# Optimization experiments

Measured on AMD Instinct MI355X. Metric: run time of the kernel, lower is better.

## Reference

```python
import jax, jax.numpy as jnp
import numpy as np

B, L, K1, P = 16, 224, 8192, 16  # batch, spectral bands, pixels, endmembers
LEAKY_SLOPE = 0.01  # torch nn.LeakyReLU default


def setup_inputs() -> dict:
    key = jax.random.key(0)
    ks = jax.random.split(key, 7)
    return {
        "a": jax.random.normal(ks[0], (B, P, K1), jnp.float32),
        "d2": jax.random.normal(ks[1], (B, P, K1), jnp.float32),
        "y": jax.random.normal(ks[2], (B, L, K1), jnp.float32),
        "w3_w": jax.random.normal(ks[3], (P, P), jnp.float32) * 0.1,  # Conv1d(P,P,1) weight squeezed
        "b3_w": jax.random.normal(ks[4], (P, P), jnp.float32) * 0.1,
        "w3_c": jax.random.normal(ks[5], (1, L, P), jnp.float32),     # kernel codebook
        "sigma": jnp.ones((1,), jnp.float32) * 2.0,
        "ca_w": jax.random.normal(ks[6], (2, P), jnp.float32) * 0.1,  # CA Conv1d(P,2,1) weight squeezed
    }


def reference(a, d2, y, w3_w, b3_w, w3_c, sigma, ca_w):
    # h2 = Conv1d(P,P,1)(a - d2)  -> pointwise matmul over channel dim
    h2 = jnp.einsum('pq,bqn->bpn', w3_w, a - d2)  # (B,P,K1)

    # GaussianKernelLayer: pairwise L2 distances between y pixels (B,L,K1)
    # and codebook columns w3_c (1,L,P), via the GEMM identity
    # ||u-v||^2 = ||u||^2 + ||v||^2 - 2 u.v  (avoids the (B,L,K1,P) broadcast).
    y_sq = jnp.sum(y * y, axis=1)            # (B,K1)
    c_sq = jnp.sum(w3_c * w3_c, axis=1)      # (1,P)
    cross = jnp.einsum('blk,olp->bkp', y, w3_c)  # (B,K1,P)
    dist_sq = jnp.maximum(y_sq[:, :, None] + c_sq[:, None, :] - 2.0 * cross, 0.0)
    dist = jnp.sqrt(dist_sq)                 # (B,K1,P)
    h3 = jnp.exp(-0.5 * jnp.square(dist / sigma[0]))
    h3 = jnp.transpose(h3, (0, 2, 1))        # (B,P,K1)

    # CA channel attention: avg/max pool over pixels -> Conv1d(P,2,1) -> LeakyReLU -> softmax
    avg = jnp.mean(h3, axis=-1)              # (B,P)
    mx = jnp.max(h3, axis=-1)                # (B,P)
    conv_lrelu = lambda v: jax.nn.leaky_relu(jnp.einsum('cp,bp->bc', ca_w, v), LEAKY_SLOPE)
    ratio = jax.nn.softmax(conv_lrelu(avg) + conv_lrelu(mx), axis=-1)  # (B,2)

    # combine center pixel + mean pixel via bmm with ratio
    mid = h3[:, :, K1 // 2]                  # (B,P)
    mean = jnp.mean(h3, axis=-1)             # (B,P)
    stacked = jnp.stack([mid, mean], axis=1)  # (B,2,P)
    comb = jnp.einsum('bc,bcp->bp', ratio, stacked)  # (B,P)

    # h4 = Conv1d(P,P,1)(comb[:, :, None])
    h4 = jnp.einsum('pq,bq->bp', b3_w, comb)[:, :, None]  # (B,P,1)

    return h4 + h2  # broadcast over pixel dim -> (B,P,K1)
```

## Files before the change

kernel.cpp:

```cpp
#include <hip/hip_runtime.h>

#define Bn  16
#define Ln  224
#define K1n 8192
#define Pn  16
#define NCHUNK 16
#define RG  16
#define NG  (Ln / RG)


__global__ __launch_bounds__(512, 2) void k_stats(
    const float* __restrict__ y,
    const float* __restrict__ w3c,
    const float* __restrict__ sigma,
    float* __restrict__ ws_sum,
    float* __restrict__ ws_max,
    float* __restrict__ ws_mid)
{
    __shared__ float s_csq_part[32][Pn];
    __shared__ float s_csq[Pn];
    __shared__ float s_part_s[8][Pn];
    __shared__ float s_part_m[8][Pn];

    const int tid   = threadIdx.x;
    const int lane  = tid & 63;
    const int wv    = tid >> 6;
    const int b     = blockIdx.x >> 4;
    const int chunk = blockIdx.x & 15;

    {
        const int p   = tid & 15;
        const int sub = tid >> 4;
        float cs = 0.f;
        for (int l = sub; l < Ln; l += 32) {
            float v = w3c[l * Pn + p];
            cs = fmaf(v, v, cs);
        }
        s_csq_part[sub][p] = cs;
    }
    __syncthreads();
    if (tid < Pn) {
        float cs = 0.f;
#pragma unroll
        for (int s = 0; s < 32; ++s) cs += s_csq_part[s][tid];
        s_csq[tid] = cs;
    }
    __syncthreads();

    float cross[Pn];
#pragma unroll
    for (int p = 0; p < Pn; ++p) cross[p] = 0.f;
    float ysq = 0.f;

    const float* yp = y + (size_t)b * Ln * K1n + (chunk << 9) + tid;

    float v[RG], vn[RG];
#pragma unroll
    for (int j = 0; j < RG; ++j) v[j] = yp[(size_t)j * K1n];

    for (int g = 0; g < NG; ++g) {
        if (g < NG - 1) {
#pragma unroll
            for (int j = 0; j < RG; ++j)
                vn[j] = yp[(size_t)((g + 1) * RG + j) * K1n];
        }
        const float* wrow = w3c + (size_t)g * RG * Pn;
#pragma unroll
        for (int j = 0; j < RG; ++j) {
            ysq = fmaf(v[j], v[j], ysq);
#pragma unroll
            for (int p = 0; p < Pn; ++p)
                cross[p] = fmaf(v[j], wrow[j * Pn + p], cross[p]);
        }
        if (g < NG - 1) {
#pragma unroll
            for (int j = 0; j < RG; ++j) v[j] = vn[j];
        }
    }

    const float sg = sigma[0];
    const float nh = -0.5f / (sg * sg);

    float h3[Pn];
#pragma unroll
    for (int p = 0; p < Pn; ++p) {
        float d = fmaxf(ysq + s_csq[p] - 2.f * cross[p], 0.f);
        h3[p] = __expf(d * nh);
    }

    if (chunk == 8 && tid == 0) {
#pragma unroll
        for (int p = 0; p < Pn; ++p) ws_mid[b * Pn + p] = h3[p];
    }

#pragma unroll
    for (int p = 0; p < Pn; ++p) {
        float s = h3[p];
        float m = h3[p];
#pragma unroll
        for (int off = 32; off > 0; off >>= 1) {
            s += __shfl_down(s, off, 64);
            m = fmaxf(m, __shfl_down(m, off, 64));
        }
        if (lane == 0) { s_part_s[wv][p] = s; s_part_m[wv][p] = m; }
    }
    __syncthreads();
    if (tid < Pn) {
        float s = 0.f, m = -1.f;
#pragma unroll
        for (int w = 0; w < 8; ++w) {
            s += s_part_s[w][tid];
            m = fmaxf(m, s_part_m[w][tid]);
        }
        const int base = (b * NCHUNK + chunk) * Pn + tid;
        ws_sum[base] = s;
        ws_max[base] = m;
    }
}

__global__ __launch_bounds__(512, 2) void k_out(
    const float* __restrict__ a,
    const float* __restrict__ d2,
    const float* __restrict__ w3w,
    const float* __restrict__ b3w,
    const float* __restrict__ caw,
    const float* __restrict__ ws_sum,
    const float* __restrict__ ws_max,
    const float* __restrict__ ws_mid,
    float* __restrict__ out)
{
    __shared__ float s_red_s[16][Pn];
    __shared__ float s_red_m[16][Pn];
    __shared__ float s_avg[Pn], s_mx[Pn], s_mid[Pn], s_h4[Pn];
    __shared__ float s_t[2];

    const int tid = threadIdx.x;
    const int b   = blockIdx.x >> 4;
    const int kb  = (blockIdx.x & 15) << 9;

    const float* ap = a  + (size_t)b * Pn * K1n + kb + tid;
    const float* dp = d2 + (size_t)b * Pn * K1n + kb + tid;
    float av[Pn], dv[Pn];
#pragma unroll
    for (int q = 0; q < Pn; ++q) av[q] = ap[(size_t)q * K1n];
#pragma unroll
    for (int q = 0; q < Pn; ++q) dv[q] = dp[(size_t)q * K1n];

    if (tid < 256) {
        const int p   = tid & 15;
        const int grp = tid >> 4;
        const int i0  = (b * NCHUNK + grp) * Pn + p;
        s_red_s[grp][p] = ws_sum[i0];
        s_red_m[grp][p] = ws_max[i0];
    }
    __syncthreads();
    if (tid < Pn) {
        float s = 0.f, m = -1.f;
#pragma unroll
        for (int g = 0; g < 16; ++g) {
            s += s_red_s[g][tid];
            m = fmaxf(m, s_red_m[g][tid]);
        }
        s_avg[tid] = s * (1.f / (float)K1n);
        s_mx[tid]  = m;
        s_mid[tid] = ws_mid[b * Pn + tid];
    }
    __syncthreads();

    if (tid < 2) {
        float t1 = 0.f, t2 = 0.f;
        for (int p = 0; p < Pn; ++p) {
            float cw = caw[tid * Pn + p];
            t1 = fmaf(cw, s_avg[p], t1);
            t2 = fmaf(cw, s_mx[p],  t2);
        }
        t1 = (t1 > 0.f) ? t1 : 0.01f * t1;
        t2 = (t2 > 0.f) ? t2 : 0.01f * t2;
        s_t[tid] = t1 + t2;
    }
    __syncthreads();

    if (tid < Pn) {
        float t0 = s_t[0], u1 = s_t[1];
        float mt = fmaxf(t0, u1);
        float e0 = __expf(t0 - mt), e1 = __expf(u1 - mt);
        float inv = 1.f / (e0 + e1);
        s_red_s[0][tid] = (e0 * inv) * s_mid[tid] + (e1 * inv) * s_avg[tid];
    }
    __syncthreads();

    if (tid < Pn) {
        float h = 0.f;
        for (int q = 0; q < Pn; ++q) h = fmaf(b3w[tid * Pn + q], s_red_s[0][q], h);
        s_h4[tid] = h;
    }
    __syncthreads();

    float diff[Pn];
#pragma unroll
    for (int q = 0; q < Pn; ++q) diff[q] = av[q] - dv[q];

    float* op = out + (size_t)b * Pn * K1n + kb + tid;
#pragma unroll
    for (int p = 0; p < Pn; ++p) {
        float h2 = s_h4[p];
#pragma unroll
        for (int q = 0; q < Pn; ++q)
            h2 = fmaf(w3w[p * Pn + q], diff[q], h2);
        op[(size_t)p * K1n] = h2;
    }
}

extern "C" void kernel_launch(void* const* d_in, const int* in_sizes, int n_in,
                              void* d_out, int out_size, void* d_ws, size_t ws_size,
                              hipStream_t stream) {
    const float* a     = (const float*)d_in[0];
    const float* d2    = (const float*)d_in[1];
    const float* y     = (const float*)d_in[2];
    const float* w3w   = (const float*)d_in[3];
    const float* b3w   = (const float*)d_in[4];
    const float* w3c   = (const float*)d_in[5];
    const float* sigma = (const float*)d_in[6];
    const float* caw   = (const float*)d_in[7];

    float* ws_sum = (float*)d_ws;
    float* ws_max = ws_sum + Bn * NCHUNK * Pn;
    float* ws_mid = ws_max + Bn * NCHUNK * Pn;

    k_stats<<<dim3(Bn * NCHUNK), dim3(512), 0, stream>>>(
        y, w3c, sigma, ws_sum, ws_max, ws_mid);

    k_out<<<dim3(Bn * NCHUNK), dim3(512), 0, stream>>>(
        a, d2, w3w, b3w, caw, ws_sum, ws_max, ws_mid, (float*)d_out);
}
```

Measured before the change: 211.8 us.

## Fuse stats and output kernels via cooperative grid sync, prefetch a/d2 early

Merges the two kernels into one cooperative kernel that syncs the grid between computing per-chunk Gaussian statistics and writing the output. The a and d2 loads are issued before the grid barrier so their latency overlaps the wait. The y streaming loop is also reworked to double-buffer two register groups in place of copying a prefetch buffer. This trades a second kernel launch for a grid-wide barrier and much higher register pressure, with launch bounds lowered to one block per multiprocessor minimum.

```diff
diff --git a/kernel.cpp b/kernel.cpp
--- a/kernel.cpp
+++ b/kernel.cpp
@@ -1,4 +1,7 @@
 #include <hip/hip_runtime.h>
+#include <hip/hip_cooperative_groups.h>
+
+namespace cg = cooperative_groups;
 
 #define Bn  16
 #define Ln  224
@@ -9,18 +12,28 @@
 #define NG  (Ln / RG)
 
 
-__global__ __launch_bounds__(512, 2) void k_stats(
+__global__ __launch_bounds__(512, 1) void k_fused(
     const float* __restrict__ y,
     const float* __restrict__ w3c,
     const float* __restrict__ sigma,
+    const float* __restrict__ a,
+    const float* __restrict__ d2,
+    const float* __restrict__ w3w,
+    const float* __restrict__ b3w,
+    const float* __restrict__ caw,
     float* __restrict__ ws_sum,
     float* __restrict__ ws_max,
-    float* __restrict__ ws_mid)
+    float* __restrict__ ws_mid,
+    float* __restrict__ out)
 {
     __shared__ float s_csq_part[32][Pn];
     __shared__ float s_csq[Pn];
     __shared__ float s_part_s[8][Pn];
     __shared__ float s_part_m[8][Pn];
+    __shared__ float s_red_s[16][Pn];
+    __shared__ float s_red_m[16][Pn];
+    __shared__ float s_avg[Pn], s_mx[Pn], s_mid[Pn], s_h4[Pn];
+    __shared__ float s_t[2];
 
     const int tid   = threadIdx.x;
     const int lane  = tid & 63;
@@ -54,27 +67,42 @@
 
     const float* yp = y + (size_t)b * Ln * K1n + (chunk << 9) + tid;
 
-    float v[RG], vn[RG];
-#pragma unroll
-    for (int j = 0; j < RG; ++j) v[j] = yp[(size_t)j * K1n];
-
-    for (int g = 0; g < NG; ++g) {
-        if (g < NG - 1) {
+    float vA[RG], vB[RG];
+#pragma unroll
+    for (int j = 0; j < RG; ++j) vA[j] = yp[(size_t)j * K1n];
+#pragma unroll
+    for (int j = 0; j < RG; ++j) vB[j] = yp[(size_t)(RG + j) * K1n];
+
+    for (int g = 0; g < NG; g += 2) {
+        {
+            const float* wrow = w3c + (size_t)g * RG * Pn;
+#pragma unroll
+            for (int j = 0; j < RG; ++j) {
+                ysq = fmaf(vA[j], vA[j], ysq);
+#pragma unroll
+                for (int p = 0; p < Pn; ++p)
+                    cross[p] = fmaf(vA[j], wrow[j * Pn + p], cross[p]);
+            }
+        }
+        if (g + 2 < NG) {
 #pragma unroll
             for (int j = 0; j < RG; ++j)
-                vn[j] = yp[(size_t)((g + 1) * RG + j) * K1n];
-        }
-        const float* wrow = w3c + (size_t)g * RG * Pn;
-#pragma unroll
-        for (int j = 0; j < RG; ++j) {
-            ysq = fmaf(v[j], v[j], ysq);
-#pragma unroll
-            for (int p = 0; p < Pn; ++p)
-                cross[p] = fmaf(v[j], wrow[j * Pn + p], cross[p]);
-        }
-        if (g < NG - 1) {
-#pragma unroll
-            for (int j = 0; j < RG; ++j) v[j] = vn[j];
+                vA[j] = yp[(size_t)((g + 2) * RG + j) * K1n];
+        }
+        {
+            const float* wrow = w3c + (size_t)(g + 1) * RG * Pn;
+#pragma unroll
+            for (int j = 0; j < RG; ++j) {
+                ysq = fmaf(vB[j], vB[j], ysq);
+#pragma unroll
+                for (int p = 0; p < Pn; ++p)
+                    cross[p] = fmaf(vB[j], wrow[j * Pn + p], cross[p]);
+            }
+        }
+        if (g + 3 < NG) {
+#pragma unroll
+            for (int j = 0; j < RG; ++j)
+                vB[j] = yp[(size_t)((g + 3) * RG + j) * K1n];
         }
     }
 
@@ -116,28 +144,8 @@
         ws_sum[base] = s;
         ws_max[base] = m;
     }
-}
-
-__global__ __launch_bounds__(512, 2) void k_out(
-    const float* __restrict__ a,
-    const float* __restrict__ d2,
-    const float* __restrict__ w3w,
-    const float* __restrict__ b3w,
-    const float* __restrict__ caw,
-    const float* __restrict__ ws_sum,
-    const float* __restrict__ ws_max,
-    const float* __restrict__ ws_mid,
-    float* __restrict__ out)
-{
-    __shared__ float s_red_s[16][Pn];
-    __shared__ float s_red_m[16][Pn];
-    __shared__ float s_avg[Pn], s_mx[Pn], s_mid[Pn], s_h4[Pn];
-    __shared__ float s_t[2];
-
-    const int tid = threadIdx.x;
-    const int b   = blockIdx.x >> 4;
-    const int kb  = (blockIdx.x & 15) << 9;
-
+
+    const int kb = chunk << 9;
     const float* ap = a  + (size_t)b * Pn * K1n + kb + tid;
     const float* dp = d2 + (size_t)b * Pn * K1n + kb + tid;
     float av[Pn], dv[Pn];
@@ -145,6 +153,9 @@
     for (int q = 0; q < Pn; ++q) av[q] = ap[(size_t)q * K1n];
 #pragma unroll
     for (int q = 0; q < Pn; ++q) dv[q] = dp[(size_t)q * K1n];
+
+    __threadfence();
+    cg::this_grid().sync();
 
     if (tid < 256) {
         const int p   = tid & 15;
@@ -226,10 +237,14 @@
     float* ws_sum = (float*)d_ws;
     float* ws_max = ws_sum + Bn * NCHUNK * Pn;
     float* ws_mid = ws_max + Bn * NCHUNK * Pn;
-
-    k_stats<<<dim3(Bn * NCHUNK), dim3(512), 0, stream>>>(
-        y, w3c, sigma, ws_sum, ws_max, ws_mid);
-
-    k_out<<<dim3(Bn * NCHUNK), dim3(512), 0, stream>>>(
-        a, d2, w3w, b3w, caw, ws_sum, ws_max, ws_mid, (float*)d_out);
+    float* outp   = (float*)d_out;
+
+    void* args[] = {
+        (void*)&y, (void*)&w3c, (void*)&sigma,
+        (void*)&a, (void*)&d2, (void*)&w3w, (void*)&b3w, (void*)&caw,
+        (void*)&ws_sum, (void*)&ws_max, (void*)&ws_mid, (void*)&outp
+    };
+    hipLaunchCooperativeKernel((const void*)k_fused,
+                               dim3(Bn * NCHUNK), dim3(512),
+                               args, 0, stream);
 }
```

Result: slower. 333.9 us (+57.6%).
